# Performance work log

Measured on AMD Instinct MI355X. Metric: run time of the kernel, lower is better.

The kernel has to match this reference:

```python
import jax, jax.numpy as jnp
import numpy as np

B, S, D = 2, 1024, 2048
H, HK, HD = 16, 4, 128
E, TOPK, I = 16, 6, 1024
IS = 2048  # shared experts intermediate = moe_intermediate_size[0] * moe_num_shared_experts
EPS = 1e-6
NORM_MIN = 1e-12
SCALE = HD ** -0.5


def setup_inputs() -> dict:
    key = jax.random.key(0)
    ks = jax.random.split(key, 16)
    w = lambda k, *sh: jax.random.normal(k, sh, jnp.float32) * 0.02
    # interleaved RoPE tables (rotate_half_text pairs even/odd dims)
    inv_freq = 1.0 / (10000.0 ** (np.arange(0, HD, 2, dtype=np.float32) / HD))
    freqs = np.outer(np.arange(S, dtype=np.float32), inv_freq)        # [S, HD/2]
    emb = np.repeat(freqs, 2, axis=-1)                                 # [S, HD]
    cos = jnp.asarray(np.broadcast_to(np.cos(emb)[None], (B, S, HD)).copy())
    sin = jnp.asarray(np.broadcast_to(np.sin(emb)[None], (B, S, HD)).copy())
    return dict(
        hidden_states=jax.random.normal(ks[0], (B, S, D), jnp.float32),
        cos=cos, sin=sin,
        ln1_w=jnp.ones((D,), jnp.float32),
        ln2_w=jnp.ones((D,), jnp.float32),
        Wq=w(ks[1], D, H * HD), Wk=w(ks[2], D, HK * HD), Wv=w(ks[3], D, HK * HD), Wo=w(ks[4], H * HD, D),
        Wgate=w(ks[5], D, E),
        corr_bias=jnp.zeros((E,), jnp.float32),
        Wg=w(ks[6], E, D, I), Wu=w(ks[7], E, D, I), Wd=w(ks[8], E, I, D),
        Wgs=w(ks[9], D, IS), Wus=w(ks[10], D, IS), Wds=w(ks[11], IS, D),
    )


def rms_norm(x, weight, eps=EPS):
    xf = x.astype(jnp.float32)
    var = jnp.mean(xf * xf, axis=-1, keepdims=True)
    return (weight * (xf * jax.lax.rsqrt(var + eps))).astype(x.dtype)


def rotate_half(x):
    # interleaved variant: (x0, x1, x2, x3, ...) -> (-x1, x0, -x3, x2, ...)
    x1 = x[..., 0::2]
    x2 = x[..., 1::2]
    return jnp.stack((-x2, x1), axis=-1).reshape(x.shape)


def apply_rope(q, k, cos, sin):
    # q: [B,H,S,HD], k: [B,HK,S,HD], cos/sin: [B,S,HD] -> unsqueeze head dim
    c = cos[:, None].astype(jnp.float32)
    s = sin[:, None].astype(jnp.float32)
    qe = (q.astype(jnp.float32) * c + rotate_half(q).astype(jnp.float32) * s).astype(q.dtype)
    ke = (k.astype(jnp.float32) * c + rotate_half(k).astype(jnp.float32) * s).astype(k.dtype)
    return qe, ke


def attention(x, cos, sin, Wq, Wk, Wv, Wo):
    b, s, _ = x.shape
    q = (x @ Wq).reshape(b, s, H, HD).transpose(0, 2, 1, 3)    # [B,H,S,HD]
    k = (x @ Wk).reshape(b, s, HK, HD).transpose(0, 2, 1, 3)   # [B,HK,S,HD]
    v = (x @ Wv).reshape(b, s, HK, HD).transpose(0, 2, 1, 3)
    q, k = apply_rope(q, k, cos, sin)
    rep = H // HK
    k = jnp.repeat(k, rep, axis=1)
    v = jnp.repeat(v, rep, axis=1)
    scores = jnp.einsum('bhqd,bhkd->bhqk', q, k).astype(jnp.float32) * SCALE
    mask = jnp.triu(jnp.full((s, s), jnp.finfo(jnp.float32).min, jnp.float32), 1)
    attn = jax.nn.softmax(scores + mask, axis=-1).astype(x.dtype)
    out = jnp.einsum('bhqk,bhkd->bhqd', attn, v)
    out = out.transpose(0, 2, 1, 3).reshape(b, s, H * HD)
    return out @ Wo


def moe(x, Wgate, corr_bias, Wg, Wu, Wd, Wgs, Wus, Wds):
    b, s, d = x.shape
    # shared experts (dense SwiGLU MLP)
    shared = (jax.nn.silu(x @ Wgs) * (x @ Wus)) @ Wds
    xt = x.reshape(-1, d)                                       # [T, D]
    T = xt.shape[0]
    logits = xt.astype(jnp.float32) @ Wgate                     # float32 gate
    probs = jax.nn.softmax(logits, axis=-1)
    _, sel = jax.lax.top_k(probs + corr_bias, TOPK)             # [T, K]
    rw = jnp.take_along_axis(probs, sel, axis=-1)               # gather un-corrected probs
    rw = rw / jnp.clip(jnp.sum(rw, axis=-1, keepdims=True), NORM_MIN)
    # dense routing matrix [T, E] (zero for unselected experts == index_add semantics)
    route = jnp.zeros((T, E), jnp.float32).at[jnp.arange(T)[:, None], sel].set(rw)
    route = route.astype(x.dtype)
    # run all experts densely, mask with routing weights
    g = jnp.einsum('td,edi->tei', xt, Wg)
    u = jnp.einsum('td,edi->tei', xt, Wu)
    eo = jnp.einsum('tei,eid->ted', jax.nn.silu(g) * u, Wd)     # per-expert down proj
    y = jnp.einsum('ted,te->td', eo, route).reshape(b, s, d)
    return y + shared


def reference(hidden_states, cos, sin, ln1_w, ln2_w, Wq, Wk, Wv, Wo,
              Wgate, corr_bias, Wg, Wu, Wd, Wgs, Wus, Wds):
    residual = hidden_states
    h = rms_norm(hidden_states, ln1_w)
    h = attention(h, cos, sin, Wq, Wk, Wv, Wo)
    h = residual + h
    residual = h
    h = rms_norm(h, ln2_w)
    h = moe(h, Wgate, corr_bias, Wg, Wu, Wd, Wgs, Wus, Wds)
    return residual + h
```

## Files before the change

### kernel.cpp

```cpp
#include <hip/hip_runtime.h>
#include <cstdint>

typedef unsigned short u16;
typedef __attribute__((ext_vector_type(8))) short short8;
typedef __attribute__((ext_vector_type(4))) short s16x4;
typedef __attribute__((ext_vector_type(4))) float f32x4;

#define MFMA_16x16x32(a,b,c) __builtin_amdgcn_mfma_f32_16x16x32_bf16(a,b,c,0,0,0)

#define GLDS16(lds, g) __builtin_amdgcn_global_load_lds( \
    (const __attribute__((address_space(1))) unsigned int*)(g), \
    (__attribute__((address_space(3))) unsigned int*)(lds), 16, 0, 0)

#define VMCNT4()  asm volatile("s_waitcnt vmcnt(4)" ::: "memory")
#define VMCNT0()  asm volatile("s_waitcnt vmcnt(0)" ::: "memory")

#define BB 2
#define SS 1024
#define DD 2048
#define HH 16
#define HKK 4
#define HDD 128
#define EE 16
#define NTOP 6
#define II 1024
#define ISS 2048
#define TT 2048
#define CAP 2048

__device__ __forceinline__ u16 f2b(float f) {
    union { float f; uint32_t u; } v; v.f = f;
    uint32_t r = v.u + 0x7FFFu + ((v.u >> 16) & 1u);
    return (u16)(r >> 16);
}
__device__ __forceinline__ float b2f(u16 h) {
    union { uint32_t u; float f; } v; v.u = ((uint32_t)h) << 16;
    return v.f;
}
__device__ __forceinline__ void fsplit(float f, u16& hi, u16& lo) {
    u16 h = f2b(f);
    hi = h;
    lo = f2b(f - b2f(h));
}

template<bool SPLIT>
__global__ __launch_bounds__(256) void k_prep(
    const float* __restrict__ In, u16* __restrict__ Oh, u16* __restrict__ Ol,
    int R, int C)
{
    const size_t zoff = (size_t)blockIdx.z * R * C;
    In += zoff; Oh += zoff; if (SPLIT) Ol += zoff;
    const int r0 = blockIdx.y * 32, c0 = blockIdx.x * 32;
    __shared__ float tile[32][33];
    const int tx = threadIdx.x & 31, ty = threadIdx.x >> 5;
    #pragma unroll
    for (int i = 0; i < 4; ++i)
        tile[ty + i*8][tx] = In[(size_t)(r0 + ty + i*8)*C + c0 + tx];
    __syncthreads();
    const int c = threadIdx.x >> 3, rs = (threadIdx.x & 7) * 4;
    s16x4 hv, lv;
    #pragma unroll
    for (int j = 0; j < 4; ++j) {
        float f = tile[rs + j][c];
        u16 hb = f2b(f);
        hv[j] = (short)hb;
        if (SPLIT) lv[j] = (short)f2b(f - b2f(hb));
        else lv[j] = 0;
    }
    *(s16x4*)(Oh + (size_t)(c0 + c)*R + r0 + rs) = hv;
    if (SPLIT) *(s16x4*)(Ol + (size_t)(c0 + c)*R + r0 + rs) = lv;
}

__global__ __launch_bounds__(256) void k_rmsnorm_split(
    const float* __restrict__ X, const float* __restrict__ Wt,
    u16* __restrict__ Oh, u16* __restrict__ Ol)
{
    const int t = blockIdx.x;
    const float* x = X + (size_t)t * DD;
    const int base = threadIdx.x * 8;
    f32x4 v0 = *(const f32x4*)(x + base);
    f32x4 v1 = *(const f32x4*)(x + base + 4);
    float ss = 0.f;
    #pragma unroll
    for (int j = 0; j < 4; ++j) ss += v0[j]*v0[j] + v1[j]*v1[j];
    #pragma unroll
    for (int o = 1; o < 64; o <<= 1) ss += __shfl_xor(ss, o);
    __shared__ float red[4];
    if ((threadIdx.x & 63) == 0) red[threadIdx.x >> 6] = ss;
    __syncthreads();
    float tot = red[0] + red[1] + red[2] + red[3];
    float inv = rsqrtf(tot * (1.0f/DD) + 1e-6f);
    f32x4 w0 = *(const f32x4*)(Wt + base);
    f32x4 w1 = *(const f32x4*)(Wt + base + 4);
    u16* oh = Oh + (size_t)t*DD + base;
    u16* ol = Ol + (size_t)t*DD + base;
    #pragma unroll
    for (int j = 0; j < 4; ++j) {
        float y0 = v0[j]*inv*w0[j];
        float y1 = v1[j]*inv*w1[j];
        fsplit(y0, oh[j],   ol[j]);
        fsplit(y1, oh[4+j], ol[4+j]);
    }
}

__global__ __launch_bounds__(256) void k_rmsnorm_bf(
    const float* __restrict__ X, const float* __restrict__ Wt,
    u16* __restrict__ Ob, float* __restrict__ Of)
{
    const int t = blockIdx.x;
    const float* x = X + (size_t)t * DD;
    const int base = threadIdx.x * 8;
    f32x4 v0 = *(const f32x4*)(x + base);
    f32x4 v1 = *(const f32x4*)(x + base + 4);
    float ss = 0.f;
    #pragma unroll
    for (int j = 0; j < 4; ++j) ss += v0[j]*v0[j] + v1[j]*v1[j];
    #pragma unroll
    for (int o = 1; o < 64; o <<= 1) ss += __shfl_xor(ss, o);
    __shared__ float red[4];
    if ((threadIdx.x & 63) == 0) red[threadIdx.x >> 6] = ss;
    __syncthreads();
    float tot = red[0] + red[1] + red[2] + red[3];
    float inv = rsqrtf(tot * (1.0f/DD) + 1e-6f);
    f32x4 w0 = *(const f32x4*)(Wt + base);
    f32x4 w1 = *(const f32x4*)(Wt + base + 4);
    u16* ob = Ob + (size_t)t*DD + base;
    float* of = Of + (size_t)t*DD + base;
    #pragma unroll
    for (int j = 0; j < 4; ++j) {
        float y0 = v0[j]*inv*w0[j];
        float y1 = v1[j]*inv*w1[j];
        ob[j] = f2b(y0); ob[4+j] = f2b(y1);
        of[j] = y0;      of[4+j] = y1;
    }
}


template<int EPI>
__global__ __launch_bounds__(256) void k8_hi(
    const u16* __restrict__ Ah, const u16* __restrict__ Al,
    const u16* __restrict__ Bth, const u16* __restrict__ Btl,
    float* __restrict__ C, const float* __restrict__ Res,
    int M, int N, int K)
{
    __shared__ u16 As[3][128][32];
    __shared__ u16 Bs[3][128][32];
    const int tid = threadIdx.x, lane = tid & 63, w = tid >> 6;
    const int m0 = blockIdx.y * 128, n0 = blockIdx.x * 128;
    const int wm = (w >> 1) * 64, wn = (w & 1) * 64;
    const int l15 = lane & 15, lhi = lane >> 4;
    f32x4 acc[4][4];
    #pragma unroll
    for (int a = 0; a < 4; ++a)
        #pragma unroll
        for (int b = 0; b < 4; ++b) acc[a][b] = 0;

    const int gr = w*32 + (lane >> 2), gc = (lane & 3) * 8;
    const u16* ahP = Ah  + (size_t)(m0 + gr) * K + gc;
    const u16* alP = Al  + (size_t)(m0 + gr) * K + gc;
    const u16* bhP = Bth + (size_t)(n0 + gr) * K + gc;
    const u16* blP = Btl + (size_t)(n0 + gr) * K + gc;
    const size_t r16 = (size_t)16 * K;
    const int ntk = K >> 5;
    const int nt = 3 * ntk;

    auto stage = [&](int bf, int t) {
        int seg = t / ntk;
        int kk = (t - seg * ntk) << 5;
        const u16* ap = (seg == 2) ? alP : ahP;
        const u16* bp = (seg == 1) ? blP : bhP;
        GLDS16(&As[bf][w*32][0],      ap + kk);
        GLDS16(&As[bf][w*32 + 16][0], ap + r16 + kk);
        GLDS16(&Bs[bf][w*32][0],      bp + kk);
        GLDS16(&Bs[bf][w*32 + 16][0], bp + r16 + kk);
    };

    stage(0, 0); stage(1, 1);
    for (int t = 0; t < nt; ++t) {
        if (t < nt - 1) VMCNT4(); else VMCNT0();
        __builtin_amdgcn_s_barrier();
        if (t + 2 < nt) stage((t + 2) % 3, t + 2);
        const int cb = t % 3;
        short8 af[4], bf4[4];
        #pragma unroll
        for (int i = 0; i < 4; ++i) {
            af[i]  = *(const short8*)&As[cb][wm + i*16 + l15][lhi*8];
            bf4[i] = *(const short8*)&Bs[cb][wn + i*16 + l15][lhi*8];
        }
        __builtin_amdgcn_s_setprio(1);
        #pragma unroll
        for (int a = 0; a < 4; ++a)
            #pragma unroll
            for (int b = 0; b < 4; ++b)
                acc[a][b] = MFMA_16x16x32(af[a], bf4[b], acc[a][b]);
        __builtin_amdgcn_s_setprio(0);
    }
    #pragma unroll
    for (int a = 0; a < 4; ++a)
      #pragma unroll
      for (int b = 0; b < 4; ++b)
        #pragma unroll
        for (int r = 0; r < 4; ++r) {
            int m = m0 + wm + a*16 + lhi*4 + r;
            int n = n0 + wn + b*16 + l15;
            size_t off = (size_t)m * N + n;
            float v = acc[a][b][r];
            if (EPI == 1) C[off] = v + Res[off];
            else C[off] = v;
        }
}

template<int EPI>
__global__ __launch_bounds__(256) void k8_gemm(
    const u16* __restrict__ A, const u16* __restrict__ Bt,
    void* __restrict__ C, int M, int N, int K)
{
    __shared__ u16 As[3][128][32];
    __shared__ u16 Bs[3][128][32];
    const int tid = threadIdx.x, lane = tid & 63, w = tid >> 6;
    const int m0 = blockIdx.y * 128, n0 = blockIdx.x * 128;
    const int wm = (w >> 1) * 64, wn = (w & 1) * 64;
    const int l15 = lane & 15, lhi = lane >> 4;
    f32x4 acc[4][4];
    #pragma unroll
    for (int a = 0; a < 4; ++a)
        #pragma unroll
        for (int b = 0; b < 4; ++b) acc[a][b] = 0;

    const int gr = w*32 + (lane >> 2), gc = (lane & 3) * 8;
    const u16* aP = A  + (size_t)(m0 + gr) * K + gc;
    const u16* bP = Bt + (size_t)(n0 + gr) * K + gc;
    const size_t r16 = (size_t)16 * K;
    const int nt = K >> 5;

    auto stage = [&](int bf, int t) {
        int kk = t << 5;
        GLDS16(&As[bf][w*32][0],      aP + kk);
        GLDS16(&As[bf][w*32 + 16][0], aP + r16 + kk);
        GLDS16(&Bs[bf][w*32][0],      bP + kk);
        GLDS16(&Bs[bf][w*32 + 16][0], bP + r16 + kk);
    };

    stage(0, 0); stage(1, 1);
    for (int t = 0; t < nt; ++t) {
        if (t < nt - 1) VMCNT4(); else VMCNT0();
        __builtin_amdgcn_s_barrier();
        if (t + 2 < nt) stage((t + 2) % 3, t + 2);
        const int cb = t % 3;
        short8 af[4], bf4[4];
        #pragma unroll
        for (int i = 0; i < 4; ++i) {
            af[i]  = *(const short8*)&As[cb][wm + i*16 + l15][lhi*8];
            bf4[i] = *(const short8*)&Bs[cb][wn + i*16 + l15][lhi*8];
        }
        __builtin_amdgcn_s_setprio(1);
        #pragma unroll
        for (int a = 0; a < 4; ++a)
            #pragma unroll
            for (int b = 0; b < 4; ++b)
                acc[a][b] = MFMA_16x16x32(af[a], bf4[b], acc[a][b]);
        __builtin_amdgcn_s_setprio(0);
    }
    #pragma unroll
    for (int a = 0; a < 4; ++a)
      #pragma unroll
      for (int b = 0; b < 4; ++b)
        #pragma unroll
        for (int r = 0; r < 4; ++r) {
            int m = m0 + wm + a*16 + lhi*4 + r;
            int n = n0 + wn + b*16 + l15;
            size_t off = (size_t)m * N + n;
            float v = acc[a][b][r];
            if (EPI == 0) ((u16*)C)[off] = f2b(v);
            else ((float*)C)[off] = v;
        }
}

template<bool GATHER>
__global__ __launch_bounds__(256) void k8_glu(
    const u16* __restrict__ Xb, const u16* __restrict__ W1t,
    const u16* __restrict__ W2t, u16* __restrict__ Hout,
    const int* __restrict__ list, const int* __restrict__ cntp,
    int M, int NE, int K)
{
    const int e = GATHER ? blockIdx.z : 0;
    const int cnt = GATHER ? cntp[e] : M;
    const int m0 = blockIdx.y * 128;
    if (m0 >= cnt) return;
    const int n0 = blockIdx.x * 64;
    const u16* w1 = W1t + (size_t)e * NE * K;
    const u16* w2 = W2t + (size_t)e * NE * K;
    u16* hout = Hout + (size_t)e * CAP * NE;
    const int* lst = GATHER ? (list + e * CAP) : nullptr;

    __shared__ u16 As[3][128][32];
    __shared__ u16 B1s[3][64][32];
    __shared__ u16 B2s[3][64][32];

    const int tid = threadIdx.x, lane = tid & 63, w = tid >> 6;
    const int wm = (w >> 1) * 64, wn = (w & 1) * 32;
    const int l15 = lane & 15, lhi = lane >> 4;
    f32x4 acc1[4][2], acc2[4][2];
    #pragma unroll
    for (int a = 0; a < 4; ++a)
        #pragma unroll
        for (int j = 0; j < 2; ++j) { acc1[a][j] = 0; acc2[a][j] = 0; }

    const int gr  = w*32 + (lane >> 2);
    const int grB = w*16 + (lane >> 2);
    const int gc  = (lane & 3) * 8;
    int arow0, arow1;
    if (GATHER) {
        int mr0 = m0 + gr, mr1 = m0 + gr + 16;
        arow0 = (mr0 < cnt) ? (lst[mr0] >> 3) : 0;
        arow1 = (mr1 < cnt) ? (lst[mr1] >> 3) : 0;
    } else { arow0 = m0 + gr; arow1 = m0 + gr + 16; }
    const u16* aP0 = Xb + (size_t)arow0 * K + gc;
    const u16* aP1 = Xb + (size_t)arow1 * K + gc;
    const u16* b1P = w1 + (size_t)(n0 + grB) * K + gc;
    const u16* b2P = w2 + (size_t)(n0 + grB) * K + gc;
    const int nt = K >> 5;

    auto stage = [&](int bf, int t) {
        int kk = t << 5;
        GLDS16(&As[bf][w*32][0],      aP0 + kk);
        GLDS16(&As[bf][w*32 + 16][0], aP1 + kk);
        GLDS16(&B1s[bf][w*16][0],     b1P + kk);
        GLDS16(&B2s[bf][w*16][0],     b2P + kk);
    };

    stage(0, 0); stage(1, 1);
    for (int t = 0; t < nt; ++t) {
        if (t < nt - 1) VMCNT4(); else VMCNT0();
        __builtin_amdgcn_s_barrier();
        if (t + 2 < nt) stage((t + 2) % 3, t + 2);
        const int cb = t % 3;
        short8 af[4], b1[2], b2[2];
        #pragma unroll
        for (int i = 0; i < 4; ++i) af[i] = *(const short8*)&As[cb][wm + i*16 + l15][lhi*8];
        #pragma unroll
        for (int j = 0; j < 2; ++j) {
            b1[j] = *(const short8*)&B1s[cb][wn + j*16 + l15][lhi*8];
            b2[j] = *(const short8*)&B2s[cb][wn + j*16 + l15][lhi*8];
        }
        __builtin_amdgcn_s_setprio(1);
        #pragma unroll
        for (int a = 0; a < 4; ++a)
            #pragma unroll
            for (int j = 0; j < 2; ++j) {
                acc1[a][j] = MFMA_16x16x32(af[a], b1[j], acc1[a][j]);
                acc2[a][j] = MFMA_16x16x32(af[a], b2[j], acc2[a][j]);
            }
        __builtin_amdgcn_s_setprio(0);
    }
    #pragma unroll
    for (int a = 0; a < 4; ++a)
      #pragma unroll
      for (int j = 0; j < 2; ++j)
        #pragma unroll
        for (int r = 0; r < 4; ++r) {
            int m = m0 + wm + a*16 + lhi*4 + r;
            if (m < cnt) {
                int n = n0 + wn + j*16 + l15;
                float g = acc1[a][j][r], u = acc2[a][j][r];
                float hval = g / (1.0f + __expf(-g)) * u;
                hout[(size_t)m * NE + n] = f2b(hval);
            }
        }
}

__global__ __launch_bounds__(256) void k8_down_scatter(
    const u16* __restrict__ Hb, const u16* __restrict__ WdTt,
    u16* __restrict__ Rbuf, const int* __restrict__ list,
    const float* __restrict__ wts, const int* __restrict__ cntp,
    int N, int K)
{
    const int e = blockIdx.z;
    const int cnt = cntp[e];
    const int m0 = blockIdx.y * 128;
    if (m0 >= cnt) return;
    const int n0 = blockIdx.x * 128;
    const u16* A  = Hb   + (size_t)e * CAP * K;
    const u16* Bt = WdTt + (size_t)e * N * K;

    __shared__ u16 As[3][128][32];
    __shared__ u16 Bs[3][128][32];
    const int tid = threadIdx.x, lane = tid & 63, w = tid >> 6;
    const int wm = (w >> 1) * 64, wn = (w & 1) * 64;
    const int l15 = lane & 15, lhi = lane >> 4;
    f32x4 acc[4][4];
    #pragma unroll
    for (int a = 0; a < 4; ++a)
        #pragma unroll
        for (int b = 0; b < 4; ++b) acc[a][b] = 0;

    const int gr = w*32 + (lane >> 2), gc = (lane & 3) * 8;
    const u16* aP = A  + (size_t)(m0 + gr) * K + gc;
    const u16* bP = Bt + (size_t)(n0 + gr) * K + gc;
    const size_t r16 = (size_t)16 * K;
    const int nt = K >> 5;

    auto stage = [&](int bf, int t) {
        int kk = t << 5;
        GLDS16(&As[bf][w*32][0],      aP + kk);
        GLDS16(&As[bf][w*32 + 16][0], aP + r16 + kk);
        GLDS16(&Bs[bf][w*32][0],      bP + kk);
        GLDS16(&Bs[bf][w*32 + 16][0], bP + r16 + kk);
    };

    stage(0, 0); stage(1, 1);
    for (int t = 0; t < nt; ++t) {
        if (t < nt - 1) VMCNT4(); else VMCNT0();
        __builtin_amdgcn_s_barrier();
        if (t + 2 < nt) stage((t + 2) % 3, t + 2);
        const int cb = t % 3;
        short8 af[4], bf4[4];
        #pragma unroll
        for (int i = 0; i < 4; ++i) {
            af[i]  = *(const short8*)&As[cb][wm + i*16 + l15][lhi*8];
            bf4[i] = *(const short8*)&Bs[cb][wn + i*16 + l15][lhi*8];
        }
        __builtin_amdgcn_s_setprio(1);
        #pragma unroll
        for (int a = 0; a < 4; ++a)
            #pragma unroll
            for (int b = 0; b < 4; ++b)
                acc[a][b] = MFMA_16x16x32(af[a], bf4[b], acc[a][b]);
        __builtin_amdgcn_s_setprio(0);
    }
    #pragma unroll
    for (int a = 0; a < 4; ++a)
      #pragma unroll
      for (int b = 0; b < 4; ++b)
        #pragma unroll
        for (int r = 0; r < 4; ++r) {
            int m = m0 + wm + a*16 + lhi*4 + r;
            if (m < cnt) {
                int n = n0 + wn + b*16 + l15;
                int enc = list[e*CAP + m];
                float wgt = wts[e*CAP + m];
                int tok = enc >> 3, kk = enc & 7;
                Rbuf[((size_t)tok*NTOP + kk)*N + n] = f2b(acc[a][b][r] * wgt);
            }
        }
}

__global__ __launch_bounds__(256) void k_rope_split(
    const float* __restrict__ QKV,
    const float* __restrict__ Cs, const float* __restrict__ Sn,
    u16* __restrict__ Qh, u16* __restrict__ Ql,
    u16* __restrict__ Kh, u16* __restrict__ Kl)
{
    int id = blockIdx.x * 256 + threadIdx.x;
    int pr = id & 63;
    int rest = id >> 6;
    int hh = rest % 20;
    int tok = rest / 20;
    if (tok >= TT) return;
    int d0 = pr * 2;
    float c0 = Cs[(size_t)tok*HDD + d0];
    float c1 = Cs[(size_t)tok*HDD + d0 + 1];
    float s0 = Sn[(size_t)tok*HDD + d0];
    float s1 = Sn[(size_t)tok*HDD + d0 + 1];
    const float* p = QKV + (size_t)tok*3072 + (hh < HH ? hh*HDD : 2048 + (hh - HH)*HDD);
    float x0 = p[d0], x1 = p[d0+1];
    float y0 = x0*c0 - x1*s0;
    float y1 = x1*c1 + x0*s1;
    u16 *oh, *ol;
    size_t ooff;
    if (hh < HH) { ooff = ((size_t)tok*HH + hh)*HDD + d0; oh = Qh; ol = Ql; }
    else         { ooff = ((size_t)tok*HKK + (hh - HH))*HDD + d0; oh = Kh; ol = Kl; }
    fsplit(y0, oh[ooff],     ol[ooff]);
    fsplit(y1, oh[ooff + 1], ol[ooff + 1]);
}

__global__ __launch_bounds__(256) void k_split_vt(
    const float* __restrict__ QKV, u16* __restrict__ Vth, u16* __restrict__ Vtl)
{
    int id = blockIdx.x * 256 + threadIdx.x;
    int oid = id * 8;
    int s0 = oid & (SS - 1);
    int r = oid >> 10;
    int d = r & (HDD - 1);
    int bh = r >> 7;
    int b = bh >> 2, hk = bh & 3;
    #pragma unroll
    for (int j = 0; j < 8; ++j) {
        int s = s0 + j;
        float v = QKV[(size_t)(b*SS + s)*3072 + 2560 + hk*HDD + d];
        fsplit(v, Vth[oid + j], Vtl[oid + j]);
    }
}

__global__ __launch_bounds__(256) void k_attn_hi(
    const u16* __restrict__ Qh, const u16* __restrict__ Ql,
    const u16* __restrict__ Kh, const u16* __restrict__ Kl,
    const u16* __restrict__ Vth, const u16* __restrict__ Vtl,
    u16* __restrict__ Oh, u16* __restrict__ Ol)
{
    const int tid = threadIdx.x;
    const int lane = tid & 63;
    const int w = tid >> 6;
    const int q0 = blockIdx.x * 64;
    const int b = blockIdx.y >> 4;
    const int h = blockIdx.y & 15;
    const int hk = h >> 2;
    const int l15 = lane & 15, lhi = lane >> 4;

    __shared__ u16 Ksh[32][136];
    __shared__ u16 Ksl[32][136];
    __shared__ u16 Vsh[128][40];
    __shared__ u16 Vsl[128][40];
    __shared__ u16 Psh[4][16][40];
    __shared__ u16 Psl[4][16][40];

    short8 qfh[4], qfl[4];
    {
        const int qrow = q0 + w*16 + l15;
        const u16* qph = Qh + ((size_t)(b*SS + qrow)*HH + h)*HDD;
        const u16* qpl = Ql + ((size_t)(b*SS + qrow)*HH + h)*HDD;
        #pragma unroll
        for (int c = 0; c < 4; ++c) {
            qfh[c] = *(const short8*)(qph + c*32 + lhi*8);
            qfl[c] = *(const short8*)(qpl + c*32 + lhi*8);
        }
    }

    f32x4 oacc[8];
    #pragma unroll
    for (int ch = 0; ch < 8; ++ch) oacc[ch] = 0;
    float m_r[4] = {-1e30f, -1e30f, -1e30f, -1e30f};
    float l_r[4] = {0.f, 0.f, 0.f, 0.f};

    const int nkt = (q0 + 64) >> 5;
    const int kr = tid >> 3, kc = (tid & 7) * 16;
    const int vd = tid >> 1, vj = (tid & 1) * 16;

    for (int kt = 0; kt < nkt; ++kt) {
        __syncthreads();
        {
            size_t koff = ((size_t)(b*SS + kt*32 + kr)*HKK + hk)*HDD + kc;
            *(short8*)&Ksh[kr][kc]     = *(const short8*)(Kh + koff);
            *(short8*)&Ksh[kr][kc + 8] = *(const short8*)(Kh + koff + 8);
            *(short8*)&Ksl[kr][kc]     = *(const short8*)(Kl + koff);
            *(short8*)&Ksl[kr][kc + 8] = *(const short8*)(Kl + koff + 8);
        }
        {
            size_t voff = ((size_t)(b*HKK + hk)*HDD + vd)*SS + kt*32 + vj;
            *(short8*)&Vsh[vd][vj]     = *(const short8*)(Vth + voff);
            *(short8*)&Vsh[vd][vj + 8] = *(const short8*)(Vth + voff + 8);
            *(short8*)&Vsl[vd][vj]     = *(const short8*)(Vtl + voff);
            *(short8*)&Vsl[vd][vj + 8] = *(const short8*)(Vtl + voff + 8);
        }
        __syncthreads();

        f32x4 s0 = 0, s1 = 0;
        #pragma unroll
        for (int c = 0; c < 4; ++c) {
            short8 kh0 = *(const short8*)&Ksh[l15][c*32 + lhi*8];
            short8 kl0 = *(const short8*)&Ksl[l15][c*32 + lhi*8];
            short8 kh1 = *(const short8*)&Ksh[16 + l15][c*32 + lhi*8];
            short8 kl1 = *(const short8*)&Ksl[16 + l15][c*32 + lhi*8];
            s0 = MFMA_16x16x32(qfh[c], kh0, s0);
            s0 = MFMA_16x16x32(qfh[c], kl0, s0);
            s0 = MFMA_16x16x32(qfl[c], kh0, s0);
            s1 = MFMA_16x16x32(qfh[c], kh1, s1);
            s1 = MFMA_16x16x32(qfh[c], kl1, s1);
            s1 = MFMA_16x16x32(qfl[c], kh1, s1);
        }
        const int irow0 = q0 + w*16 + lhi*4;
        const int j0 = kt*32 + l15;
        float ef[4];
        #pragma unroll
        for (int r = 0; r < 4; ++r) {
            float a0 = s0[r] * 0.08838834764831845f;
            float a1 = s1[r] * 0.08838834764831845f;
            const int ir = irow0 + r;
            if (j0 > ir) a0 = -1e30f;
            if (j0 + 16 > ir) a1 = -1e30f;
            float mx = fmaxf(a0, a1);
            #pragma unroll
            for (int o = 1; o < 16; o <<= 1) mx = fmaxf(mx, __shfl_xor(mx, o));
            float mn = fmaxf(m_r[r], mx);
            ef[r] = __expf(m_r[r] - mn);
            m_r[r] = mn;
            float p0 = __expf(a0 - mn);
            float p1 = __expf(a1 - mn);
            float ps = p0 + p1;
            #pragma unroll
            for (int o = 1; o < 16; o <<= 1) ps += __shfl_xor(ps, o);
            l_r[r] = l_r[r]*ef[r] + ps;
            fsplit(p0, Psh[w][lhi*4 + r][l15],      Psl[w][lhi*4 + r][l15]);
            fsplit(p1, Psh[w][lhi*4 + r][16 + l15], Psl[w][lhi*4 + r][16 + l15]);
        }
        #pragma unroll
        for (int ch = 0; ch < 8; ++ch) {
            f32x4 t = oacc[ch];
            t[0] *= ef[0]; t[1] *= ef[1]; t[2] *= ef[2]; t[3] *= ef[3];
            oacc[ch] = t;
        }
        __syncthreads();
        short8 pah = *(const short8*)&Psh[w][l15][lhi*8];
        short8 pal = *(const short8*)&Psl[w][l15][lhi*8];
        #pragma unroll
        for (int ch = 0; ch < 8; ++ch) {
            short8 bvh = *(const short8*)&Vsh[ch*16 + l15][lhi*8];
            short8 bvl = *(const short8*)&Vsl[ch*16 + l15][lhi*8];
            oacc[ch] = MFMA_16x16x32(pah, bvh, oacc[ch]);
            oacc[ch] = MFMA_16x16x32(pah, bvl, oacc[ch]);
            oacc[ch] = MFMA_16x16x32(pal, bvh, oacc[ch]);
        }
    }
    #pragma unroll
    for (int r = 0; r < 4; ++r) {
        const int row = q0 + w*16 + lhi*4 + r;
        const float inv = 1.0f / l_r[r];
        u16* oph = Oh + ((size_t)(b*SS + row)*HH + h)*HDD;
        u16* opl = Ol + ((size_t)(b*SS + row)*HH + h)*HDD;
        #pragma unroll
        for (int ch = 0; ch < 8; ++ch) {
            float o = oacc[ch][r] * inv;
            fsplit(o, oph[ch*16 + l15], opl[ch*16 + l15]);
        }
    }
}

__global__ __launch_bounds__(256) void k_router(
    const float* __restrict__ X, const float* __restrict__ Wg,
    const float* __restrict__ bias,
    int* __restrict__ cnt, int* __restrict__ list, float* __restrict__ wts)
{
    const int t = blockIdx.x;
    const int e = threadIdx.x & 15, sl = threadIdx.x >> 4;
    const float* x = X + (size_t)t * DD;
    float part = 0.f;
    for (int i = 0; i < 128; ++i) {
        int k = sl * 128 + i;
        part += x[k] * Wg[(size_t)k * EE + e];
    }
    __shared__ float red[16][17];
    red[sl][e] = part;
    __syncthreads();
    if (threadIdx.x == 0) {
        float lg[16], pr[16];
        for (int ee = 0; ee < 16; ++ee) {
            float s = 0.f;
            for (int q = 0; q < 16; ++q) s += red[q][ee];
            lg[ee] = s;
        }
        float mx = lg[0];
        for (int ee = 1; ee < 16; ++ee) mx = fmaxf(mx, lg[ee]);
        float sum = 0.f;
        for (int ee = 0; ee < 16; ++ee) { pr[ee] = expf(lg[ee] - mx); sum += pr[ee]; }
        float isum = 1.0f / sum;
        for (int ee = 0; ee < 16; ++ee) pr[ee] *= isum;
        unsigned used = 0;
        int sel[NTOP]; float rw[NTOP]; float s6 = 0.f;
        for (int kk = 0; kk < NTOP; ++kk) {
            int best = 0; float bv = -1e30f;
            for (int ee = 0; ee < 16; ++ee) {
                if (used & (1u << ee)) continue;
                float sc = pr[ee] + bias[ee];
                if (sc > bv) { bv = sc; best = ee; }
            }
            used |= 1u << best;
            sel[kk] = best; rw[kk] = pr[best]; s6 += pr[best];
        }
        float inv6 = 1.0f / fmaxf(s6, 1e-12f);
        for (int kk = 0; kk < NTOP; ++kk) {
            int ee = sel[kk];
            int pos = atomicAdd(&cnt[ee], 1);
            list[ee*CAP + pos] = (t << 3) | kk;
            wts[ee*CAP + pos] = rw[kk] * inv6;
        }
    }
}

__global__ __launch_bounds__(256) void k_final(
    const float* __restrict__ h2, const float* __restrict__ yb,
    const u16* __restrict__ rb, float* __restrict__ out)
{
    int id = blockIdx.x * 256 + threadIdx.x;
    size_t i4 = (size_t)id * 4;
    int t = id >> 9;
    int d = (id & 511) * 4;
    f32x4 acc = *(const f32x4*)(h2 + i4);
    f32x4 y = *(const f32x4*)(yb + i4);
    acc += y;
    #pragma unroll
    for (int kk = 0; kk < NTOP; ++kk) {
        s16x4 rv = *(const s16x4*)(rb + ((size_t)t*NTOP + kk)*DD + d);
        acc[0] += b2f((u16)rv[0]); acc[1] += b2f((u16)rv[1]);
        acc[2] += b2f((u16)rv[2]); acc[3] += b2f((u16)rv[3]);
    }
    *(f32x4*)(out + i4) = acc;
}

extern "C" void kernel_launch(void* const* d_in, const int* in_sizes, int n_in,
                              void* d_out, int out_size, void* d_ws, size_t ws_size,
                              hipStream_t stream)
{
    (void)in_sizes; (void)n_in; (void)out_size; (void)ws_size;
    const float* hidden = (const float*)d_in[0];
    const float* cosb   = (const float*)d_in[1];
    const float* sinb   = (const float*)d_in[2];
    const float* ln1    = (const float*)d_in[3];
    const float* ln2    = (const float*)d_in[4];
    const float* Wq     = (const float*)d_in[5];
    const float* Wk     = (const float*)d_in[6];
    const float* Wv     = (const float*)d_in[7];
    const float* Wo     = (const float*)d_in[8];
    const float* Wgate  = (const float*)d_in[9];
    const float* cbias  = (const float*)d_in[10];
    const float* Wg     = (const float*)d_in[11];
    const float* Wu     = (const float*)d_in[12];
    const float* Wd     = (const float*)d_in[13];
    const float* Wgs    = (const float*)d_in[14];
    const float* Wus    = (const float*)d_in[15];
    const float* Wds    = (const float*)d_in[16];
    float* out = (float*)d_out;

    char* ws = (char*)d_ws;
    size_t off = 0;
    auto alloc = [&](size_t bytes) {
        void* p = ws + off;
        off = (off + bytes + 255) & ~(size_t)255;
        return p;
    };
    u16* WqkvTh = (u16*)alloc((size_t)3072*2048*2);
    u16* WqkvTl = (u16*)alloc((size_t)3072*2048*2);
    u16* WoTh   = (u16*)alloc((size_t)2048*2048*2);
    u16* WoTl   = (u16*)alloc((size_t)2048*2048*2);
    u16* WgsT   = (u16*)alloc((size_t)2048*2048*2);
    u16* WusT   = (u16*)alloc((size_t)2048*2048*2);
    u16* WdsT   = (u16*)alloc((size_t)2048*2048*2);
    u16* WgT    = (u16*)alloc((size_t)EE*II*DD*2);
    u16* WuT    = (u16*)alloc((size_t)EE*II*DD*2);
    u16* WdT    = (u16*)alloc((size_t)EE*DD*II*2);
    u16*   x1h  = (u16*)  alloc((size_t)TT*DD*2);
    u16*   x1l  = (u16*)  alloc((size_t)TT*DD*2);
    float* qkvf = (float*)alloc((size_t)TT*3072*4);
    u16*   qh   = (u16*)  alloc((size_t)TT*HH*HDD*2);
    u16*   ql   = (u16*)  alloc((size_t)TT*HH*HDD*2);
    u16*   kh   = (u16*)  alloc((size_t)TT*HKK*HDD*2);
    u16*   kl   = (u16*)  alloc((size_t)TT*HKK*HDD*2);
    u16*   vth  = (u16*)  alloc((size_t)TT*HKK*HDD*2);
    u16*   vtl  = (u16*)  alloc((size_t)TT*HKK*HDD*2);
    u16*   aoh  = (u16*)  alloc((size_t)TT*HH*HDD*2);
    u16*   aol  = (u16*)  alloc((size_t)TT*HH*HDD*2);
    float* h2   = (float*)alloc((size_t)TT*DD*4);
    u16*   x2   = (u16*)  alloc((size_t)TT*DD*2);
    float* x2f  = (float*)alloc((size_t)TT*DD*4);
    int*   cnt  = (int*)  alloc(256);
    int*   lst  = (int*)  alloc((size_t)EE*CAP*4);
    float* wts  = (float*)alloc((size_t)EE*CAP*4);
    u16*   hE   = (u16*)  alloc((size_t)EE*CAP*II*2);
    u16*   rbuf = (u16*)  alloc((size_t)TT*NTOP*DD*2);
    u16*   hs   = x1h;
    float* ybuf = qkvf;

    k_prep<true ><<<dim3(64,64,1), 256, 0, stream>>>(Wq, WqkvTh, WqkvTl, 2048, 2048);
    k_prep<true ><<<dim3(16,64,1), 256, 0, stream>>>(Wk, WqkvTh + (size_t)2048*2048, WqkvTl + (size_t)2048*2048, 2048, 512);
    k_prep<true ><<<dim3(16,64,1), 256, 0, stream>>>(Wv, WqkvTh + (size_t)2560*2048, WqkvTl + (size_t)2560*2048, 2048, 512);
    k_prep<true ><<<dim3(64,64,1), 256, 0, stream>>>(Wo, WoTh, WoTl, 2048, 2048);
    k_prep<false><<<dim3(64,64,1), 256, 0, stream>>>(Wgs, WgsT, nullptr, 2048, 2048);
    k_prep<false><<<dim3(64,64,1), 256, 0, stream>>>(Wus, WusT, nullptr, 2048, 2048);
    k_prep<false><<<dim3(64,64,1), 256, 0, stream>>>(Wds, WdsT, nullptr, 2048, 2048);
    k_prep<false><<<dim3(32,64,EE), 256, 0, stream>>>(Wg, WgT, nullptr, 2048, 1024);
    k_prep<false><<<dim3(32,64,EE), 256, 0, stream>>>(Wu, WuT, nullptr, 2048, 1024);
    k_prep<false><<<dim3(64,32,EE), 256, 0, stream>>>(Wd, WdT, nullptr, 1024, 2048);

    k_rmsnorm_split<<<TT, 256, 0, stream>>>(hidden, ln1, x1h, x1l);
    k8_hi<2><<<dim3(24,16), 256, 0, stream>>>(x1h, x1l, WqkvTh, WqkvTl, qkvf, nullptr, TT, 3072, DD);
    k_rope_split<<<(TT*20*64)/256, 256, 0, stream>>>(qkvf, cosb, sinb, qh, ql, kh, kl);
    k_split_vt<<<(TT*HKK*HDD/8)/256, 256, 0, stream>>>(qkvf, vth, vtl);
    k_attn_hi<<<dim3(SS/64, BB*HH), 256, 0, stream>>>(qh, ql, kh, kl, vth, vtl, aoh, aol);
    k8_hi<1><<<dim3(16,16), 256, 0, stream>>>(aoh, aol, WoTh, WoTl, h2, hidden, TT, DD, HH*HDD);

    k_rmsnorm_bf<<<TT, 256, 0, stream>>>(h2, ln2, x2, x2f);
    (void)hipMemsetAsync(cnt, 0, 256, stream);
    k_router<<<TT, 256, 0, stream>>>(x2f, Wgate, cbias, cnt, lst, wts);
    k8_glu<false><<<dim3(ISS/64, TT/128, 1), 256, 0, stream>>>(x2, WgsT, WusT, hs, nullptr, nullptr, TT, ISS, DD);
    k8_gemm<2><<<dim3(16,16), 256, 0, stream>>>(hs, WdsT, ybuf, TT, DD, ISS);
    k8_glu<true><<<dim3(II/64, CAP/128, EE), 256, 0, stream>>>(x2, WgT, WuT, hE, lst, cnt, CAP, II, DD);
    k8_down_scatter<<<dim3(DD/128, CAP/128, EE), 256, 0, stream>>>(hE, WdT, rbuf, lst, wts, cnt, DD, II);
    k_final<<<(TT*DD/4)/256, 256, 0, stream>>>(h2, ybuf, rbuf, out);
}
```

Baseline: 1.188 ms.

## Fuse split-bf16 hi/lo passes into one K loop and enlarge MoE GEMM tiles

```diff
diff --git a/kernel.cpp b/kernel.cpp
--- a/kernel.cpp
+++ b/kernel.cpp
@@ -12,7 +12,8 @@
     (const __attribute__((address_space(1))) unsigned int*)(g), \
     (__attribute__((address_space(3))) unsigned int*)(lds), 16, 0, 0)
 
-#define VMCNT4()  asm volatile("s_waitcnt vmcnt(4)" ::: "memory")
+#define VMCNT8()  asm volatile("s_waitcnt vmcnt(8)" ::: "memory")
+#define VMCNT6()  asm volatile("s_waitcnt vmcnt(6)" ::: "memory")
 #define VMCNT0()  asm volatile("s_waitcnt vmcnt(0)" ::: "memory")
 
 #define BB 2
@@ -135,7 +136,6 @@
     }
 }
 
-
 template<int EPI>
 __global__ __launch_bounds__(256) void k8_hi(
     const u16* __restrict__ Ah, const u16* __restrict__ Al,
@@ -143,8 +143,10 @@
     float* __restrict__ C, const float* __restrict__ Res,
     int M, int N, int K)
 {
-    __shared__ u16 As[3][128][32];
-    __shared__ u16 Bs[3][128][32];
+    __shared__ u16 Ash[2][128][32];
+    __shared__ u16 Asl[2][128][32];
+    __shared__ u16 Bsh[2][128][32];
+    __shared__ u16 Bsl[2][128][32];
     const int tid = threadIdx.x, lane = tid & 63, w = tid >> 6;
     const int m0 = blockIdx.y * 128, n0 = blockIdx.x * 128;
     const int wm = (w >> 1) * 64, wn = (w & 1) * 64;
@@ -161,39 +163,45 @@
     const u16* bhP = Bth + (size_t)(n0 + gr) * K + gc;
     const u16* blP = Btl + (size_t)(n0 + gr) * K + gc;
     const size_t r16 = (size_t)16 * K;
-    const int ntk = K >> 5;
-    const int nt = 3 * ntk;
+    const int nt = K >> 5;
 
     auto stage = [&](int bf, int t) {
-        int seg = t / ntk;
-        int kk = (t - seg * ntk) << 5;
-        const u16* ap = (seg == 2) ? alP : ahP;
-        const u16* bp = (seg == 1) ? blP : bhP;
-        GLDS16(&As[bf][w*32][0],      ap + kk);
-        GLDS16(&As[bf][w*32 + 16][0], ap + r16 + kk);
-        GLDS16(&Bs[bf][w*32][0],      bp + kk);
-        GLDS16(&Bs[bf][w*32 + 16][0], bp + r16 + kk);
+        int kk = t << 5;
+        GLDS16(&Ash[bf][w*32][0],      ahP + kk);
+        GLDS16(&Ash[bf][w*32 + 16][0], ahP + r16 + kk);
+        GLDS16(&Asl[bf][w*32][0],      alP + kk);
+        GLDS16(&Asl[bf][w*32 + 16][0], alP + r16 + kk);
+        GLDS16(&Bsh[bf][w*32][0],      bhP + kk);
+        GLDS16(&Bsh[bf][w*32 + 16][0], bhP + r16 + kk);
+        GLDS16(&Bsl[bf][w*32][0],      blP + kk);
+        GLDS16(&Bsl[bf][w*32 + 16][0], blP + r16 + kk);
     };
 
-    stage(0, 0); stage(1, 1);
+    stage(0, 0);
     for (int t = 0; t < nt; ++t) {
-        if (t < nt - 1) VMCNT4(); else VMCNT0();
+        if (t + 1 < nt) { stage((t + 1) & 1, t + 1); VMCNT8(); }
+        else VMCNT0();
         __builtin_amdgcn_s_barrier();
-        if (t + 2 < nt) stage((t + 2) % 3, t + 2);
-        const int cb = t % 3;
-        short8 af[4], bf4[4];
+        const int cb = t & 1;
+        short8 afh[4], afl[4], bfh[4], bfl[4];
         #pragma unroll
         for (int i = 0; i < 4; ++i) {
-            af[i]  = *(const short8*)&As[cb][wm + i*16 + l15][lhi*8];
-            bf4[i] = *(const short8*)&Bs[cb][wn + i*16 + l15][lhi*8];
+            afh[i] = *(const short8*)&Ash[cb][wm + i*16 + l15][lhi*8];
+            afl[i] = *(const short8*)&Asl[cb][wm + i*16 + l15][lhi*8];
+            bfh[i] = *(const short8*)&Bsh[cb][wn + i*16 + l15][lhi*8];
+            bfl[i] = *(const short8*)&Bsl[cb][wn + i*16 + l15][lhi*8];
         }
         __builtin_amdgcn_s_setprio(1);
         #pragma unroll
         for (int a = 0; a < 4; ++a)
             #pragma unroll
-            for (int b = 0; b < 4; ++b)
-                acc[a][b] = MFMA_16x16x32(af[a], bf4[b], acc[a][b]);
+            for (int b = 0; b < 4; ++b) {
+                acc[a][b] = MFMA_16x16x32(afh[a], bfh[b], acc[a][b]);
+                acc[a][b] = MFMA_16x16x32(afh[a], bfl[b], acc[a][b]);
+                acc[a][b] = MFMA_16x16x32(afl[a], bfh[b], acc[a][b]);
+            }
         __builtin_amdgcn_s_setprio(0);
+        __builtin_amdgcn_s_barrier();
     }
     #pragma unroll
     for (int a = 0; a < 4; ++a)
@@ -216,20 +224,22 @@
     void* __restrict__ C, int M, int N, int K)
 {
     __shared__ u16 As[3][128][32];
-    __shared__ u16 Bs[3][128][32];
+    __shared__ u16 Bs[3][256][32];
     const int tid = threadIdx.x, lane = tid & 63, w = tid >> 6;
-    const int m0 = blockIdx.y * 128, n0 = blockIdx.x * 128;
-    const int wm = (w >> 1) * 64, wn = (w & 1) * 64;
+    const int m0 = blockIdx.y * 128, n0 = blockIdx.x * 256;
+    const int wm = (w >> 1) * 64, wn = (w & 1) * 128;
     const int l15 = lane & 15, lhi = lane >> 4;
-    f32x4 acc[4][4];
+    f32x4 acc[4][8];
     #pragma unroll
     for (int a = 0; a < 4; ++a)
         #pragma unroll
-        for (int b = 0; b < 4; ++b) acc[a][b] = 0;
-
-    const int gr = w*32 + (lane >> 2), gc = (lane & 3) * 8;
-    const u16* aP = A  + (size_t)(m0 + gr) * K + gc;
-    const u16* bP = Bt + (size_t)(n0 + gr) * K + gc;
+        for (int b = 0; b < 8; ++b) acc[a][b] = 0;
+
+    const int grA = w*32 + (lane >> 2);
+    const int grB = w*64 + (lane >> 2);
+    const int gc  = (lane & 3) * 8;
+    const u16* aP = A  + (size_t)(m0 + grA) * K + gc;
+    const u16* bP = Bt + (size_t)(n0 + grB) * K + gc;
     const size_t r16 = (size_t)16 * K;
     const int nt = K >> 5;
 
@@ -237,34 +247,35 @@
         int kk = t << 5;
         GLDS16(&As[bf][w*32][0],      aP + kk);
         GLDS16(&As[bf][w*32 + 16][0], aP + r16 + kk);
-        GLDS16(&Bs[bf][w*32][0],      bP + kk);
-        GLDS16(&Bs[bf][w*32 + 16][0], bP + r16 + kk);
+        GLDS16(&Bs[bf][w*64][0],      bP + kk);
+        GLDS16(&Bs[bf][w*64 + 16][0], bP + r16 + kk);
+        GLDS16(&Bs[bf][w*64 + 32][0], bP + 2*r16 + kk);
+        GLDS16(&Bs[bf][w*64 + 48][0], bP + 3*r16 + kk);
     };
 
     stage(0, 0); stage(1, 1);
     for (int t = 0; t < nt; ++t) {
-        if (t < nt - 1) VMCNT4(); else VMCNT0();
+        if (t < nt - 1) VMCNT6(); else VMCNT0();
         __builtin_amdgcn_s_barrier();
         if (t + 2 < nt) stage((t + 2) % 3, t + 2);
         const int cb = t % 3;
-        short8 af[4], bf4[4];
-        #pragma unroll
-        for (int i = 0; i < 4; ++i) {
-            af[i]  = *(const short8*)&As[cb][wm + i*16 + l15][lhi*8];
-            bf4[i] = *(const short8*)&Bs[cb][wn + i*16 + l15][lhi*8];
-        }
+        short8 af[4], bf4[8];
+        #pragma unroll
+        for (int i = 0; i < 4; ++i) af[i] = *(const short8*)&As[cb][wm + i*16 + l15][lhi*8];
+        #pragma unroll
+        for (int i = 0; i < 8; ++i) bf4[i] = *(const short8*)&Bs[cb][wn + i*16 + l15][lhi*8];
         __builtin_amdgcn_s_setprio(1);
         #pragma unroll
         for (int a = 0; a < 4; ++a)
             #pragma unroll
-            for (int b = 0; b < 4; ++b)
+            for (int b = 0; b < 8; ++b)
                 acc[a][b] = MFMA_16x16x32(af[a], bf4[b], acc[a][b]);
         __builtin_amdgcn_s_setprio(0);
     }
     #pragma unroll
     for (int a = 0; a < 4; ++a)
       #pragma unroll
-      for (int b = 0; b < 4; ++b)
+      for (int b = 0; b < 8; ++b)
         #pragma unroll
         for (int r = 0; r < 4; ++r) {
             int m = m0 + wm + a*16 + lhi*4 + r;
@@ -287,28 +298,27 @@
     const int cnt = GATHER ? cntp[e] : M;
     const int m0 = blockIdx.y * 128;
     if (m0 >= cnt) return;
-    const int n0 = blockIdx.x * 64;
+    const int n0 = blockIdx.x * 128;
     const u16* w1 = W1t + (size_t)e * NE * K;
     const u16* w2 = W2t + (size_t)e * NE * K;
     u16* hout = Hout + (size_t)e * CAP * NE;
     const int* lst = GATHER ? (list + e * CAP) : nullptr;
 
     __shared__ u16 As[3][128][32];
-    __shared__ u16 B1s[3][64][32];
-    __shared__ u16 B2s[3][64][32];
+    __shared__ u16 B1s[3][128][32];
+    __shared__ u16 B2s[3][128][32];
 
     const int tid = threadIdx.x, lane = tid & 63, w = tid >> 6;
-    const int wm = (w >> 1) * 64, wn = (w & 1) * 32;
+    const int wm = (w >> 1) * 64, wn = (w & 1) * 64;
     const int l15 = lane & 15, lhi = lane >> 4;
-    f32x4 acc1[4][2], acc2[4][2];
+    f32x4 acc1[4][4], acc2[4][4];
     #pragma unroll
     for (int a = 0; a < 4; ++a)
         #pragma unroll
-        for (int j = 0; j < 2; ++j) { acc1[a][j] = 0; acc2[a][j] = 0; }
-
-    const int gr  = w*32 + (lane >> 2);
-    const int grB = w*16 + (lane >> 2);
-    const int gc  = (lane & 3) * 8;
+        for (int j = 0; j < 4; ++j) { acc1[a][j] = 0; acc2[a][j] = 0; }
+
+    const int gr = w*32 + (lane >> 2);
+    const int gc = (lane & 3) * 8;
     int arow0, arow1;
     if (GATHER) {
         int mr0 = m0 + gr, mr1 = m0 + gr + 16;
@@ -317,37 +327,39 @@
     } else { arow0 = m0 + gr; arow1 = m0 + gr + 16; }
     const u16* aP0 = Xb + (size_t)arow0 * K + gc;
     const u16* aP1 = Xb + (size_t)arow1 * K + gc;
-    const u16* b1P = w1 + (size_t)(n0 + grB) * K + gc;
-    const u16* b2P = w2 + (size_t)(n0 + grB) * K + gc;
+    const u16* b1P = w1 + (size_t)(n0 + gr) * K + gc;
+    const u16* b2P = w2 + (size_t)(n0 + gr) * K + gc;
+    const size_t r16 = (size_t)16 * K;
     const int nt = K >> 5;
 
     auto stage = [&](int bf, int t) {
         int kk = t << 5;
-        GLDS16(&As[bf][w*32][0],      aP0 + kk);
-        GLDS16(&As[bf][w*32 + 16][0], aP1 + kk);
-        GLDS16(&B1s[bf][w*16][0],     b1P + kk);
-        GLDS16(&B2s[bf][w*16][0],     b2P + kk);
+        GLDS16(&As[bf][w*32][0],       aP0 + kk);
+        GLDS16(&As[bf][w*32 + 16][0],  aP1 + kk);
+        GLDS16(&B1s[bf][w*32][0],      b1P + kk);
+        GLDS16(&B1s[bf][w*32 + 16][0], b1P + r16 + kk);
+        GLDS16(&B2s[bf][w*32][0],      b2P + kk);
+        GLDS16(&B2s[bf][w*32 + 16][0], b2P + r16 + kk);
     };
 
     stage(0, 0); stage(1, 1);
     for (int t = 0; t < nt; ++t) {
-        if (t < nt - 1) VMCNT4(); else VMCNT0();
+        if (t < nt - 1) VMCNT6(); else VMCNT0();
         __builtin_amdgcn_s_barrier();
         if (t + 2 < nt) stage((t + 2) % 3, t + 2);
         const int cb = t % 3;
-        short8 af[4], b1[2], b2[2];
-        #pragma unroll
-        for (int i = 0; i < 4; ++i) af[i] = *(const short8*)&As[cb][wm + i*16 + l15][lhi*8];
-        #pragma unroll
-        for (int j = 0; j < 2; ++j) {
-            b1[j] = *(const short8*)&B1s[cb][wn + j*16 + l15][lhi*8];
-            b2[j] = *(const short8*)&B2s[cb][wn + j*16 + l15][lhi*8];
+        short8 af[4], b1[4], b2[4];
+        #pragma unroll
+        for (int i = 0; i < 4; ++i) {
+            af[i] = *(const short8*)&As[cb][wm + i*16 + l15][lhi*8];
+            b1[i] = *(const short8*)&B1s[cb][wn + i*16 + l15][lhi*8];
+            b2[i] = *(const short8*)&B2s[cb][wn + i*16 + l15][lhi*8];
         }
         __builtin_amdgcn_s_setprio(1);
         #pragma unroll
         for (int a = 0; a < 4; ++a)
             #pragma unroll
-            for (int j = 0; j < 2; ++j) {
+            for (int j = 0; j < 4; ++j) {
                 acc1[a][j] = MFMA_16x16x32(af[a], b1[j], acc1[a][j]);
                 acc2[a][j] = MFMA_16x16x32(af[a], b2[j], acc2[a][j]);
             }
@@ -356,7 +368,7 @@
     #pragma unroll
     for (int a = 0; a < 4; ++a)
       #pragma unroll
-      for (int j = 0; j < 2; ++j)
+      for (int j = 0; j < 4; ++j)
         #pragma unroll
         for (int r = 0; r < 4; ++r) {
             int m = m0 + wm + a*16 + lhi*4 + r;
@@ -379,24 +391,26 @@
     const int cnt = cntp[e];
     const int m0 = blockIdx.y * 128;
     if (m0 >= cnt) return;
-    const int n0 = blockIdx.x * 128;
+    const int n0 = blockIdx.x * 256;
     const u16* A  = Hb   + (size_t)e * CAP * K;
     const u16* Bt = WdTt + (size_t)e * N * K;
 
     __shared__ u16 As[3][128][32];
-    __shared__ u16 Bs[3][128][32];
+    __shared__ u16 Bs[3][256][32];
     const int tid = threadIdx.x, lane = tid & 63, w = tid >> 6;
-    const int wm = (w >> 1) * 64, wn = (w & 1) * 64;
+    const int wm = (w >> 1) * 64, wn = (w & 1) * 128;
     const int l15 = lane & 15, lhi = lane >> 4;
-    f32x4 acc[4][4];
+    f32x4 acc[4][8];
     #pragma unroll
     for (int a = 0; a < 4; ++a)
         #pragma unroll
-        for (int b = 0; b < 4; ++b) acc[a][b] = 0;
-
-    const int gr = w*32 + (lane >> 2), gc = (lane & 3) * 8;
-    const u16* aP = A  + (size_t)(m0 + gr) * K + gc;
-    const u16* bP = Bt + (size_t)(n0 + gr) * K + gc;
+        for (int b = 0; b < 8; ++b) acc[a][b] = 0;
+
+    const int grA = w*32 + (lane >> 2);
+    const int grB = w*64 + (lane >> 2);
+    const int gc  = (lane & 3) * 8;
+    const u16* aP = A  + (size_t)(m0 + grA) * K + gc;
+    const u16* bP = Bt + (size_t)(n0 + grB) * K + gc;
     const size_t r16 = (size_t)16 * K;
     const int nt = K >> 5;
 
@@ -404,34 +418,35 @@
         int kk = t << 5;
         GLDS16(&As[bf][w*32][0],      aP + kk);
         GLDS16(&As[bf][w*32 + 16][0], aP + r16 + kk);
-        GLDS16(&Bs[bf][w*32][0],      bP + kk);
-        GLDS16(&Bs[bf][w*32 + 16][0], bP + r16 + kk);
+        GLDS16(&Bs[bf][w*64][0],      bP + kk);
+        GLDS16(&Bs[bf][w*64 + 16][0], bP + r16 + kk);
+        GLDS16(&Bs[bf][w*64 + 32][0], bP + 2*r16 + kk);
+        GLDS16(&Bs[bf][w*64 + 48][0], bP + 3*r16 + kk);
     };
 
     stage(0, 0); stage(1, 1);
     for (int t = 0; t < nt; ++t) {
-        if (t < nt - 1) VMCNT4(); else VMCNT0();
+        if (t < nt - 1) VMCNT6(); else VMCNT0();
         __builtin_amdgcn_s_barrier();
         if (t + 2 < nt) stage((t + 2) % 3, t + 2);
         const int cb = t % 3;
-        short8 af[4], bf4[4];
-        #pragma unroll
-        for (int i = 0; i < 4; ++i) {
-            af[i]  = *(const short8*)&As[cb][wm + i*16 + l15][lhi*8];
-            bf4[i] = *(const short8*)&Bs[cb][wn + i*16 + l15][lhi*8];
-        }
+        short8 af[4], bf4[8];
+        #pragma unroll
+        for (int i = 0; i < 4; ++i) af[i] = *(const short8*)&As[cb][wm + i*16 + l15][lhi*8];
+        #pragma unroll
+        for (int i = 0; i < 8; ++i) bf4[i] = *(const short8*)&Bs[cb][wn + i*16 + l15][lhi*8];
         __builtin_amdgcn_s_setprio(1);
         #pragma unroll
         for (int a = 0; a < 4; ++a)
             #pragma unroll
-            for (int b = 0; b < 4; ++b)
+            for (int b = 0; b < 8; ++b)
                 acc[a][b] = MFMA_16x16x32(af[a], bf4[b], acc[a][b]);
         __builtin_amdgcn_s_setprio(0);
     }
     #pragma unroll
     for (int a = 0; a < 4; ++a)
       #pragma unroll
-      for (int b = 0; b < 4; ++b)
+      for (int b = 0; b < 8; ++b)
         #pragma unroll
         for (int r = 0; r < 4; ++r) {
             int m = m0 + wm + a*16 + lhi*4 + r;
@@ -780,9 +795,9 @@
     k_rmsnorm_bf<<<TT, 256, 0, stream>>>(h2, ln2, x2, x2f);
     (void)hipMemsetAsync(cnt, 0, 256, stream);
     k_router<<<TT, 256, 0, stream>>>(x2f, Wgate, cbias, cnt, lst, wts);
-    k8_glu<false><<<dim3(ISS/64, TT/128, 1), 256, 0, stream>>>(x2, WgsT, WusT, hs, nullptr, nullptr, TT, ISS, DD);
-    k8_gemm<2><<<dim3(16,16), 256, 0, stream>>>(hs, WdsT, ybuf, TT, DD, ISS);
-    k8_glu<true><<<dim3(II/64, CAP/128, EE), 256, 0, stream>>>(x2, WgT, WuT, hE, lst, cnt, CAP, II, DD);
-    k8_down_scatter<<<dim3(DD/128, CAP/128, EE), 256, 0, stream>>>(hE, WdT, rbuf, lst, wts, cnt, DD, II);
+    k8_glu<false><<<dim3(ISS/128, TT/128, 1), 256, 0, stream>>>(x2, WgsT, WusT, hs, nullptr, nullptr, TT, ISS, DD);
+    k8_gemm<2><<<dim3(DD/256, TT/128), 256, 0, stream>>>(hs, WdsT, ybuf, TT, DD, ISS);
+    k8_glu<true><<<dim3(II/128, CAP/128, EE), 256, 0, stream>>>(x2, WgT, WuT, hE, lst, cnt, CAP, II, DD);
+    k8_down_scatter<<<dim3(DD/256, CAP/128, EE), 256, 0, stream>>>(hE, WdT, rbuf, lst, wts, cnt, DD, II);
     k_final<<<(TT*DD/4)/256, 256, 0, stream>>>(h2, ybuf, rbuf, out);
 }
```

New measurement: 1.491 ms. 1.25x slower.
